# Optimization experiments

Hardware: AMD Instinct MI355X
Metric: run time of the kernel (lower is better)

Reference implementation:

```python
import jax, jax.numpy as jnp
import numpy as np

B, SEQ, VOCAB = 128, 200, 1400
D = 256          # input_size == hidden_size
H = 256
NCLS = 128


def _p(key, shape, scale=0.05):
    return jax.random.normal(key, shape, dtype=jnp.float32) * scale


def setup_inputs() -> dict:
    key = jax.random.key(0)
    ks = jax.random.split(key, 24)
    inp = {
        "inputs": jax.random.uniform(ks[0], (B, SEQ, VOCAB), dtype=jnp.float32),
        "timestamps": jax.random.uniform(ks[1], (B, SEQ), dtype=jnp.float32),
        "emb": _p(ks[2], (VOCAB, D)),
        # TimeLSTM 1
        "Wall1_w": _p(ks[3], (4 * H, D)), "Wall1_b": _p(ks[4], (4 * H,)),
        "Uall1_w": _p(ks[5], (4 * H, H)), "Uall1_b": _p(ks[6], (4 * H,)),
        "Wd1_w": _p(ks[7], (H, H)), "Wd1_b": _p(ks[8], (H,)),
        # TimeLSTM 2
        "Wall2_w": _p(ks[9], (4 * H, D)), "Wall2_b": _p(ks[10], (4 * H,)),
        "Uall2_w": _p(ks[11], (4 * H, H)), "Uall2_b": _p(ks[12], (4 * H,)),
        "Wd2_w": _p(ks[13], (H, H)), "Wd2_b": _p(ks[14], (H,)),
        # attention / output heads
        "wa_w": _p(ks[15], (1, H)),
        "Wb_w": _p(ks[16], (H, H)),
        "Wout_w": _p(ks[17], (NCLS, H)),
        # initial states (torch.randn in original forward)
        "h01": jax.random.normal(ks[18], (B, H), dtype=jnp.float32),
        "c01": jax.random.normal(ks[19], (B, H), dtype=jnp.float32),
        "h02": jax.random.normal(ks[20], (B, H), dtype=jnp.float32),
        "c02": jax.random.normal(ks[21], (B, H), dtype=jnp.float32),
    }
    return inp


def _time_lstm(embedded, timestamps, h0, c0, Wall_w, Wall_b, Uall_w, Uall_b, Wd_w, Wd_b):
    # Precompute the input projection for all steps (one big GEMM).
    # NOTE: original code applies W_all to h and U_all to x.
    ux = jnp.einsum('bsd,ed->sbe', embedded, Uall_w) + Uall_b  # [seq, b, 4h]
    ts = jnp.swapaxes(timestamps, 0, 1)[:, :, None]            # [seq, b, 1]

    def step(carry, xs):
        h, c = carry
        ux_s, t_s = xs
        c_s1 = jnp.tanh(c @ Wd_w.T + Wd_b)
        c_adj = c - c_s1 + c_s1 * t_s
        gates = jax.nn.sigmoid(h @ Wall_w.T + Wall_b + ux_s)   # all 4 gates sigmoid (incl. c_tmp)
        f, i, o, c_tmp = jnp.split(gates, 4, axis=1)
        c_new = f * c_adj + i * c_tmp
        h_new = o * jnp.tanh(c_new)
        return (h_new, c_new), h_new

    _, hs = jax.lax.scan(step, (h0, c0), (ux, ts))
    return jnp.swapaxes(hs, 0, 1)  # [b, seq, h]


def reference(inputs, timestamps, emb,
              Wall1_w, Wall1_b, Uall1_w, Uall1_b, Wd1_w, Wd1_b,
              Wall2_w, Wall2_b, Uall2_w, Uall2_b, Wd2_w, Wd2_b,
              wa_w, Wb_w, Wout_w, h01, c01, h02, c02):
    embedded = jnp.einsum('bsv,vd->bsd', inputs, emb)  # [b, seq, d]
    out1 = _time_lstm(embedded, timestamps, h01, c01,
                      Wall1_w, Wall1_b, Uall1_w, Uall1_b, Wd1_w, Wd1_b)
    E = jnp.einsum('bsh,h->bs', out1, wa_w[0])
    alpha = jax.nn.softmax(E, axis=1)                  # [b, seq]
    out2 = _time_lstm(embedded, timestamps, h02, c02,
                      Wall2_w, Wall2_b, Uall2_w, Uall2_b, Wd2_w, Wd2_b)
    Beta = jnp.tanh(jnp.einsum('bsh,kh->bsk', out2, Wb_w))  # [b, seq, h]
    ctx = jnp.sum(embedded * Beta * alpha[:, :, None], axis=1)  # [b, h]
    return ctx @ Wout_w.T  # [b, num_classes]
```

## Files before the change

kernel.cpp:

```cpp
#include <hip/hip_runtime.h>

typedef unsigned short u16;
typedef unsigned long long u64;
typedef __attribute__((ext_vector_type(8))) short bf16x8;
typedef __attribute__((ext_vector_type(4))) float f32x4;
typedef __attribute__((ext_vector_type(4))) unsigned short us4;

#define MFMA(a,b,c) __builtin_amdgcn_mfma_f32_16x16x32_bf16((a),(b),(c),0,0,0)
#define KEEP(x) asm volatile("" : "+v"(x))


static __device__ __forceinline__ u16 f2b(float f){
  unsigned u = __float_as_uint(f);
  u += 0x7fffu + ((u >> 16) & 1u);
  return (u16)(u >> 16);
}
static __device__ __forceinline__ float sigm(float x){ return 1.0f/(1.0f+__expf(-x)); }
static __device__ __forceinline__ float tanhx(float x){
  x = fminf(fmaxf(x, -15.f), 15.f);
  float e = __expf(-2.f*x);
  return (1.f - e)/(1.f + e);
}
static __device__ __forceinline__ void gl16(const void* g, void* l){
  __builtin_amdgcn_global_load_lds((const __attribute__((address_space(1))) void*)g,
                                   (__attribute__((address_space(3))) void*)l, 16, 0, 0);
}

__global__ __launch_bounds__(256) void k_prep(
  const float* __restrict__ in0, u16* __restrict__ A0,
  const float* __restrict__ emb, u16* __restrict__ embT,
  const float* __restrict__ s0, const float* __restrict__ s1, const float* __restrict__ s2,
  const float* __restrict__ s3, const float* __restrict__ s4, const float* __restrict__ s5,
  const float* __restrict__ s6,
  u16* __restrict__ d0, u16* __restrict__ d1, u16* __restrict__ d2, u16* __restrict__ d3,
  u16* __restrict__ d4, u16* __restrict__ d5, u16* __restrict__ d6)
{
  int bx = blockIdx.x, tid = threadIdx.x;
  if (bx < 35200){
    long long i4 = (long long)bx*256 + tid;
    long long o = i4*4;
    int r = (int)(o / 1408);
    int c = (int)(o % 1408);
    us4 d;
    if (c + 4 <= 1400){
      f32x4 v = *(const f32x4*)&in0[(long long)r*1400 + c];
      d[0]=f2b(v[0]); d[1]=f2b(v[1]); d[2]=f2b(v[2]); d[3]=f2b(v[3]);
    } else {
      for (int k=0;k<4;k++){ int cc=c+k; d[k] = (cc<1400)? f2b(in0[(long long)r*1400+cc]) : (u16)0; }
    }
    *(us4*)&A0[(long long)r*1408 + c] = d;
  } else if (bx < 36608){
    int idx = (bx-35200)*256 + tid;
    int n = idx / 1408, k = idx % 1408;
    embT[idx] = (k < 1400) ? f2b(emb[(long long)k*256 + n]) : (u16)0;
  } else {
    long long q = (long long)(bx-36608)*256 + tid;
    const float* src; u16* dst; long long rel;
    if      (q < 65536)  { src=s0; dst=d0; rel=q; }
    else if (q < 131072) { src=s1; dst=d1; rel=q-65536; }
    else if (q < 196608) { src=s2; dst=d2; rel=q-131072; }
    else if (q < 262144) { src=s3; dst=d3; rel=q-196608; }
    else if (q < 278528) { src=s4; dst=d4; rel=q-262144; }
    else if (q < 294912) { src=s5; dst=d5; rel=q-278528; }
    else                 { src=s6; dst=d6; rel=q-294912; }
    long long o = rel*4;
    f32x4 v = *(const f32x4*)&src[o];
    us4 d; d[0]=f2b(v[0]); d[1]=f2b(v[1]); d[2]=f2b(v[2]); d[3]=f2b(v[3]);
    *(us4*)&dst[o] = d;
  }
}

__global__ __launch_bounds__(256) void k_init(float* __restrict__ E, float* __restrict__ ctx){
  int i = blockIdx.x*256 + threadIdx.x;
  if (i < 25600) E[i] = 0.f;
  else ctx[i-25600] = 0.f;
}

template<int EPI>
__global__ __launch_bounds__(256) void k_gemm(const u16* __restrict__ A, const u16* __restrict__ Bt,
    int N, int K,
    float* __restrict__ Cf, u16* __restrict__ Cb,
    const float* __restrict__ bias1, const float* __restrict__ bias2,
    const u16* __restrict__ Bt2, float* __restrict__ Cf2,
    const float* __restrict__ bias3, const float* __restrict__ bias4,
    const float* __restrict__ emb, const float* __restrict__ alpha)
{
  __shared__ __align__(16) u16 As[128*64];
  __shared__ __align__(16) u16 Bs[128*64];
  __shared__ float red[2][128];
  const int tid = threadIdx.x;
  const int l = tid & 63, w = tid >> 6;
  const int quad = l >> 4, lb = l & 15;
  const int wr = w >> 1, wc = w & 1;
  const long long m0 = (long long)blockIdx.x * 128;
  int n0 = blockIdx.y * 128;
  if (EPI==4 && blockIdx.y >= 8){
    Bt = Bt2; Cf = Cf2; bias1 = bias3; bias2 = bias4; n0 = (blockIdx.y-8)*128;
  }

  f32x4 acc[4][4];
  #pragma unroll
  for (int i=0;i<4;i++)
    #pragma unroll
    for (int j=0;j<4;j++) acc[i][j] = (f32x4){0.f,0.f,0.f,0.f};

  for (int kk = 0; kk < K; kk += 64){
    #pragma unroll
    for (int it=0; it<4; ++it){
      int slot = it*256 + tid;
      int m = slot >> 3;
      int q = (slot & 7) ^ (m & 7);
      gl16(A + (m0+m)*K + kk + q*8, &As[slot*8]);
    }
    #pragma unroll
    for (int it=0; it<4; ++it){
      int slot = it*256 + tid;
      int m = slot >> 3;
      int q = (slot & 7) ^ (m & 7);
      gl16(Bt + (long long)(n0+m)*K + kk + q*8, &Bs[slot*8]);
    }
    __syncthreads();
    #pragma unroll
    for (int ks=0; ks<2; ++ks){
      int kq = quad + ks*4;
      bf16x8 af[4], bfr[4];
      #pragma unroll
      for (int i=0;i<4;i++){ int m = wr*64 + i*16 + lb; af[i]  = *(const bf16x8*)&As[m*64 + ((kq ^ (m&7))*8)]; }
      #pragma unroll
      for (int j=0;j<4;j++){ int n = wc*64 + j*16 + lb; bfr[j] = *(const bf16x8*)&Bs[n*64 + ((kq ^ (n&7))*8)]; }
      #pragma unroll
      for (int i=0;i<4;i++)
        #pragma unroll
        for (int j=0;j<4;j++)
          acc[i][j] = MFMA(af[i], bfr[j], acc[i][j]);
    }
    __syncthreads();
  }

  if (EPI==5){
    const int b0 = (int)(m0 / 200);
    red[tid>>7][tid&127] = 0.f;
    __syncthreads();
    #pragma unroll
    for (int i=0;i<4;i++){
      #pragma unroll
      for (int j=0;j<4;j++){
        int col = wc*64 + j*16 + lb;
        #pragma unroll
        for (int r=0;r<4;r++){
          long long row = m0 + wr*64 + i*16 + quad*4 + r;
          long long o = row*N + n0 + col;
          float v = emb[o] * tanhx(acc[i][j][r]) * alpha[row];
          atomicAdd(&red[(int)(row/200) - b0][col], v);
        }
      }
    }
    __syncthreads();
    int bl = tid >> 7, col = tid & 127;
    int bb = b0 + bl;
    if (bb < 128) atomicAdd(&Cf[bb*256 + n0 + col], red[bl][col]);
    return;
  }

  #pragma unroll
  for (int i=0;i<4;i++){
    #pragma unroll
    for (int j=0;j<4;j++){
      int col = n0 + wc*64 + j*16 + lb;
      #pragma unroll
      for (int r=0;r<4;r++){
        long long row = m0 + wr*64 + i*16 + quad*4 + r;
        long long o = row*N + col;
        float v = acc[i][j][r];
        if (EPI==1){ Cf[o]=v; Cb[o]=f2b(v); }
        else { Cf[o] = v + bias1[col] + bias2[col]; }
      }
    }
  }
}

__global__ __launch_bounds__(256,1) void k_scan(
  const u16* __restrict__ Wall1, const u16* __restrict__ Wd1, const float* __restrict__ Wd1b,
  const float* __restrict__ ux1, const float* __restrict__ h01, const float* __restrict__ c01,
  const u16* __restrict__ Wall2, const u16* __restrict__ Wd2, const float* __restrict__ Wd2b,
  const float* __restrict__ ux2, const float* __restrict__ h02, const float* __restrict__ c02,
  const float* __restrict__ ts, const float* __restrict__ wa,
  float* __restrict__ E, u16* __restrict__ out2,
  u16* __restrict__ hx, u16* __restrict__ cx, int* __restrict__ seqw)
{
  __shared__ __align__(16) u16 hb[16][264];
  __shared__ __align__(16) u16 cb[16][264];
  const int bi = blockIdx.x;
  const int lstm = bi >> 5;
  const int bc   = (bi >> 2) & 7;
  const int jw   = bi & 3;
  const int grp  = bi >> 2;
  const u16* Wall  = lstm ? Wall2 : Wall1;
  const u16* Wd    = lstm ? Wd2   : Wd1;
  const float* Wdb = lstm ? Wd2b  : Wd1b;
  const float* ux  = lstm ? ux2   : ux1;
  const float* h0  = lstm ? h02   : h01;
  const float* c0  = lstm ? c02   : c01;

  const int tid = threadIdx.x;
  const int l = tid & 63, w = tid >> 6;
  const int quad = l >> 4, lb = l & 15;
  const int bg = bc*16 + lb;
  const int jwave = jw*64 + w*16;
  const int jlane = jwave + quad*4;
  const int bb = tid >> 4, jj = tid & 15, j0 = jj*16;
  const int wjw = jj >> 2;

  bf16x8 wfA[4][8], wdA[8];
  #pragma unroll
  for (int g=0; g<4; ++g)
    #pragma unroll
    for (int kk=0; kk<8; ++kk){
      wfA[g][kk] = *(const bf16x8*)&Wall[(long long)(g*256 + jwave + lb)*256 + kk*32 + quad*8];
      KEEP(wfA[g][kk]);
    }
  #pragma unroll
  for (int kk=0; kk<8; ++kk){
    wdA[kk] = *(const bf16x8*)&Wd[(long long)(jwave + lb)*256 + kk*32 + quad*8];
    KEEP(wdA[kk]);
  }

  f32x4 bcs  = *(const f32x4*)&Wdb[jlane];
  f32x4 wav  = *(const f32x4*)&wa[jlane];
  f32x4 creg = *(const f32x4*)&c0[(long long)bg*256 + jlane];

  {
    #pragma unroll
    for (int kq=0; kq<4; ++kq){
      f32x4 hv = *(const f32x4*)&h0[(long long)(bc*16+bb)*256 + j0 + kq*4];
      f32x4 cv = *(const f32x4*)&c0[(long long)(bc*16+bb)*256 + j0 + kq*4];
      us4 hp, cp;
      #pragma unroll
      for (int r=0;r<4;++r){ hp[r]=f2b(hv[r]); cp[r]=f2b(cv[r]); }
      *(us4*)&hb[bb][j0+kq*4] = hp;
      *(us4*)&cb[bb][j0+kq*4] = cp;
    }
  }
  __syncthreads();

  f32x4 uxr[4];
  #pragma unroll
  for (int g=0; g<4; ++g)
    uxr[g] = *(const f32x4*)&ux[(long long)bg*200*1024 + g*256 + jlane];
  float tcur = ts[(long long)bg*200];

  for (int s=0; s<200; ++s){
    f32x4 ad = bcs;
    #pragma unroll
    for (int kk=0;kk<8;++kk){
      bf16x8 cf = *(const bf16x8*)&cb[lb][kk*32 + quad*8];
      ad = MFMA(wdA[kk], cf, ad);
    }
    f32x4 ag[4];
    #pragma unroll
    for (int g=0; g<4; ++g) ag[g] = uxr[g];
    #pragma unroll
    for (int kk=0;kk<8;++kk){
      bf16x8 hf = *(const bf16x8*)&hb[lb][kk*32 + quad*8];
      #pragma unroll
      for (int g=0; g<4; ++g) ag[g] = MFMA(wfA[g][kk], hf, ag[g]);
    }
    f32x4 hn; us4 hp, cp;
    #pragma unroll
    for (int r=0;r<4;++r){
      float cs1 = tanhx(ad[r]);
      float cadj = creg[r] + cs1*(tcur - 1.0f);
      float fg = sigm(ag[0][r]);
      float ig = sigm(ag[1][r]);
      float og = sigm(ag[2][r]);
      float cg = sigm(ag[3][r]);
      float cn = fg*cadj + ig*cg;
      float hv = og*tanhx(cn);
      creg[r]=cn; hn[r]=hv;
      hp[r]=f2b(hv); cp[r]=f2b(cn);
    }
    if (lstm==0){
      float e = hn[0]*wav[0] + hn[1]*wav[1] + hn[2]*wav[2] + hn[3]*wav[3];
      e += __shfl_xor(e, 16, 64);
      e += __shfl_xor(e, 32, 64);
      if (l < 16) atomicAdd(&E[(long long)bg*200 + s], e);
    } else {
      *(us4*)&out2[((long long)bg*200 + s)*256 + jlane] = hp;
    }
    if (s < 199){
      const int slot = (s+1)&1;
      u64 hv64, cv64;
      __builtin_memcpy(&hv64,&hp,8); __builtin_memcpy(&cv64,&cp,8);
      long long xbase = ((long long)(slot*16 + grp)*16 + lb)*256 + jlane;
      __hip_atomic_store((u64*)&hx[xbase], hv64, __ATOMIC_RELAXED, __HIP_MEMORY_SCOPE_AGENT);
      __hip_atomic_store((u64*)&cx[xbase], cv64, __ATOMIC_RELAXED, __HIP_MEMORY_SCOPE_AGENT);
      __syncthreads();
      if (tid == 0)
        __hip_atomic_store(&seqw[(slot*16+grp)*4 + jw], s+1, __ATOMIC_RELAXED, __HIP_MEMORY_SCOPE_AGENT);
      #pragma unroll
      for (int g=0; g<4; ++g)
        uxr[g] = *(const f32x4*)&ux[((long long)bg*200 + s+1)*1024 + g*256 + jlane];
      float tnext = ts[(long long)bg*200 + s+1];
      *(us4*)&hb[lb][jlane] = hp;
      *(us4*)&cb[lb][jlane] = cp;
      if (wjw != jw){
        const int* sp = &seqw[(slot*16+grp)*4 + wjw];
        while (__hip_atomic_load(sp, __ATOMIC_RELAXED, __HIP_MEMORY_SCOPE_AGENT) != s+1)
          __builtin_amdgcn_s_sleep(1);
        long long rbase = ((long long)(slot*16 + grp)*16 + bb)*256 + j0;
        u64 hvv[4], cvv[4];
        #pragma unroll
        for (int kq=0;kq<4;++kq){
          hvv[kq] = __hip_atomic_load((const u64*)&hx[rbase + kq*4], __ATOMIC_RELAXED, __HIP_MEMORY_SCOPE_AGENT);
          cvv[kq] = __hip_atomic_load((const u64*)&cx[rbase + kq*4], __ATOMIC_RELAXED, __HIP_MEMORY_SCOPE_AGENT);
        }
        #pragma unroll
        for (int kq=0;kq<4;++kq){
          *(u64*)&hb[bb][j0+kq*4] = hvv[kq];
          *(u64*)&cb[bb][j0+kq*4] = cvv[kq];
        }
      }
      tcur = tnext;
      __syncthreads();
    }
  }
}

__global__ __launch_bounds__(256) void k_attn(const float* __restrict__ E, float* __restrict__ alpha){
  __shared__ float buf[256];
  int b = blockIdx.x, tid = threadIdx.x;
  float Ev = (tid < 200) ? E[(long long)b*200 + tid] : -1e30f;
  buf[tid]=Ev; __syncthreads();
  for (int st=128; st>0; st>>=1){ if (tid<st) buf[tid]=fmaxf(buf[tid],buf[tid+st]); __syncthreads(); }
  float mx = buf[0]; __syncthreads();
  float e = (tid<200)? __expf(Ev-mx) : 0.f;
  buf[tid]=e; __syncthreads();
  for (int st=128; st>0; st>>=1){ if (tid<st) buf[tid]+=buf[tid+st]; __syncthreads(); }
  float sm = buf[0];
  if (tid<200) alpha[(long long)b*200+tid] = e/sm;
}

__global__ __launch_bounds__(128) void k_out(const float* __restrict__ ctx, const float* __restrict__ Wout,
                                             float* __restrict__ out){
  __shared__ float cs[256];
  int b = blockIdx.x, t = threadIdx.x;
  cs[t] = ctx[b*256+t]; cs[t+128] = ctx[b*256+t+128];
  __syncthreads();
  const float* wr = Wout + (long long)t*256;
  float a0=0,a1=0,a2=0,a3=0;
  for (int j=0;j<256;j+=4){
    f32x4 v = *(const f32x4*)&wr[j];
    a0+=v[0]*cs[j]; a1+=v[1]*cs[j+1]; a2+=v[2]*cs[j+2]; a3+=v[3]*cs[j+3];
  }
  out[(long long)b*128 + t] = (a0+a1)+(a2+a3);
}

extern "C" void kernel_launch(void* const* d_in, const int* in_sizes, int n_in,
                              void* d_out, int out_size, void* d_ws, size_t ws_size,
                              hipStream_t stream)
{
  (void)in_sizes; (void)n_in; (void)out_size; (void)ws_size;
  const float* inputs = (const float*)d_in[0];
  const float* tstamp = (const float*)d_in[1];
  const float* emb    = (const float*)d_in[2];
  const float* Wall1w = (const float*)d_in[3];
  const float* Wall1b = (const float*)d_in[4];
  const float* Uall1w = (const float*)d_in[5];
  const float* Uall1b = (const float*)d_in[6];
  const float* Wd1w   = (const float*)d_in[7];
  const float* Wd1b   = (const float*)d_in[8];
  const float* Wall2w = (const float*)d_in[9];
  const float* Wall2b = (const float*)d_in[10];
  const float* Uall2w = (const float*)d_in[11];
  const float* Uall2b = (const float*)d_in[12];
  const float* Wd2w   = (const float*)d_in[13];
  const float* Wd2b   = (const float*)d_in[14];
  const float* wa     = (const float*)d_in[15];
  const float* Wbw    = (const float*)d_in[16];
  const float* Woutw  = (const float*)d_in[17];
  const float* h01    = (const float*)d_in[18];
  const float* c01    = (const float*)d_in[19];
  const float* h02    = (const float*)d_in[20];
  const float* c02    = (const float*)d_in[21];

  char* ws = (char*)d_ws;
  float* ux1   = (float*)(ws + 0);
  float* ux2   = (float*)(ws + 104857600LL);
  float* embF  = (float*)(ws + 209715200LL);
  u16*   embB  = (u16*)  (ws + 235929600LL);
  char*  scr   =          ws + 249036800LL;
  u16*   A0    = (u16*)scr;
  u16*   out2  = (u16*)  (scr + 0);
  float* alpha = (float*)(scr + 39321600LL);
  float* ctx   = (float*)(scr + 39424000LL);
  float* E     = (float*)(scr + 39555072LL);
  u16*   hx    = (u16*)  (scr + 39657472LL);
  u16*   cx    = (u16*)  (scr + 39919616LL);
  int*   seqw  = (int*)  (scr + 40181760LL);
  u16* embT    = (u16*)(ws + 321126400LL);
  u16* Wall1B  = (u16*)(ws + 321847296LL);
  u16* Wall2B  = (u16*)(ws + 322371584LL);
  u16* Uall1B  = (u16*)(ws + 322895872LL);
  u16* Uall2B  = (u16*)(ws + 323420160LL);
  u16* Wd1B    = (u16*)(ws + 323944448LL);
  u16* Wd2B    = (u16*)(ws + 324075520LL);
  u16* WbB     = (u16*)(ws + 324206592LL);

  k_prep<<<37824, 256, 0, stream>>>(inputs, A0, emb, embT,
                                    Wall1w, Wall2w, Uall1w, Uall2w, Wd1w, Wd2w, Wbw,
                                    Wall1B, Wall2B, Uall1B, Uall2B, Wd1B, Wd2B, WbB);
  k_gemm<1><<<dim3(200,2), 256, 0, stream>>>(A0, embT, 256, 1408, embF, embB,
                                             nullptr, nullptr, nullptr, nullptr,
                                             nullptr, nullptr, nullptr, nullptr);
  k_gemm<4><<<dim3(200,16), 256, 0, stream>>>(embB, Uall1B, 1024, 256, ux1, nullptr,
                                              Uall1b, Wall1b,
                                              Uall2B, ux2, Uall2b, Wall2b,
                                              nullptr, nullptr);
  k_init<<<228, 256, 0, stream>>>(E, ctx);
  k_scan<<<64, 256, 0, stream>>>(Wall1B, Wd1B, Wd1b, ux1, h01, c01,
                                 Wall2B, Wd2B, Wd2b, ux2, h02, c02,
                                 tstamp, wa, E, out2, hx, cx, seqw);
  k_attn<<<128, 256, 0, stream>>>(E, alpha);
  k_gemm<5><<<dim3(200,2), 256, 0, stream>>>(out2, WbB, 256, 256, ctx, nullptr,
                                             nullptr, nullptr, nullptr, nullptr,
                                             nullptr, nullptr, embF, alpha);
  k_out<<<128, 128, 0, stream>>>(ctx, Woutw, (float*)d_out);
}
```

Measured before the change: 1.140 ms.

## Place scan blocks by XCD for local-cache exchange and store ux in bf16

The scan kernel now reads each block's XCC ID and assigns batch groups so that the four cooperating blocks share an XCD when possible. Those blocks exchange h and c state through workgroup-scope atomics that stay in the local L2, with a bounded spin that falls back to an agent-scope mirror. The ux projections are written in bf16 with biases folded in, which halves that traffic, and the next step's ux is prefetched earlier in the loop. The aim is lower per-step cross-block synchronisation latency in the 200-step recurrence. The cost is extra atomics, duplicated payload writes, and reliance on XCD co-residency and on cache-scope behaviour that is not guaranteed.

```diff
diff --git a/kernel.cpp b/kernel.cpp
--- a/kernel.cpp
+++ b/kernel.cpp
@@ -14,6 +14,9 @@
   unsigned u = __float_as_uint(f);
   u += 0x7fffu + ((u >> 16) & 1u);
   return (u16)(u >> 16);
+}
+static __device__ __forceinline__ float b2f(u16 v){
+  return __uint_as_float(((unsigned)v) << 16);
 }
 static __device__ __forceinline__ float sigm(float x){ return 1.0f/(1.0f+__expf(-x)); }
 static __device__ __forceinline__ float tanhx(float x){
@@ -70,10 +73,12 @@
   }
 }
 
-__global__ __launch_bounds__(256) void k_init(float* __restrict__ E, float* __restrict__ ctx){
+__global__ __launch_bounds__(256) void k_init(float* __restrict__ E, float* __restrict__ ctx,
+                                              int* __restrict__ cnts){
   int i = blockIdx.x*256 + threadIdx.x;
-  if (i < 25600) E[i] = 0.f;
-  else ctx[i-25600] = 0.f;
+  if (i < 32768) E[i] = 0.f;
+  else if (i < 65536) ctx[i-32768] = 0.f;
+  else if (i < 65568) cnts[i-65536] = 0;
 }
 
 template<int EPI>
@@ -81,7 +86,7 @@
     int N, int K,
     float* __restrict__ Cf, u16* __restrict__ Cb,
     const float* __restrict__ bias1, const float* __restrict__ bias2,
-    const u16* __restrict__ Bt2, float* __restrict__ Cf2,
+    const u16* __restrict__ Bt2, u16* __restrict__ Cb2,
     const float* __restrict__ bias3, const float* __restrict__ bias4,
     const float* __restrict__ emb, const float* __restrict__ alpha)
 {
@@ -94,8 +99,8 @@
   const int wr = w >> 1, wc = w & 1;
   const long long m0 = (long long)blockIdx.x * 128;
   int n0 = blockIdx.y * 128;
-  if (EPI==4 && blockIdx.y >= 8){
-    Bt = Bt2; Cf = Cf2; bias1 = bias3; bias2 = bias4; n0 = (blockIdx.y-8)*128;
+  if (EPI==6 && blockIdx.y >= 8){
+    Bt = Bt2; Cb = Cb2; bias1 = bias3; bias2 = bias4; n0 = (blockIdx.y-8)*128;
   }
 
   f32x4 acc[4][4];
@@ -173,7 +178,7 @@
         long long o = row*N + col;
         float v = acc[i][j][r];
         if (EPI==1){ Cf[o]=v; Cb[o]=f2b(v); }
-        else { Cf[o] = v + bias1[col] + bias2[col]; }
+        else if (EPI==6){ Cb[o] = f2b(v + bias1[col] + bias2[col]); }
       }
     }
   }
@@ -181,28 +186,61 @@
 
 __global__ __launch_bounds__(256,1) void k_scan(
   const u16* __restrict__ Wall1, const u16* __restrict__ Wd1, const float* __restrict__ Wd1b,
-  const float* __restrict__ ux1, const float* __restrict__ h01, const float* __restrict__ c01,
+  const u16* __restrict__ ux1, const float* __restrict__ h01, const float* __restrict__ c01,
   const u16* __restrict__ Wall2, const u16* __restrict__ Wd2, const float* __restrict__ Wd2b,
-  const float* __restrict__ ux2, const float* __restrict__ h02, const float* __restrict__ c02,
+  const u16* __restrict__ ux2, const float* __restrict__ h02, const float* __restrict__ c02,
   const float* __restrict__ ts, const float* __restrict__ wa,
   float* __restrict__ E, u16* __restrict__ out2,
-  u16* __restrict__ hx, u16* __restrict__ cx, int* __restrict__ seqw)
+  u64* __restrict__ pay, unsigned* __restrict__ flg,
+  u64* __restrict__ mpay, unsigned* __restrict__ mflg,
+  int* __restrict__ cntp, int* __restrict__ totalp, int* __restrict__ fbp)
 {
   __shared__ __align__(16) u16 hb[16][264];
   __shared__ __align__(16) u16 cb[16][264];
+  __shared__ int bcast[3];
+  __shared__ int lok;
+
   const int bi = blockIdx.x;
   const int lstm = bi >> 5;
-  const int bc   = (bi >> 2) & 7;
-  const int jw   = bi & 3;
-  const int grp  = bi >> 2;
+  const int tid = threadIdx.x;
+
+  if (tid == 0){
+    int xcd;
+    asm volatile("s_getreg_b32 %0, hwreg(HW_REG_XCC_ID)" : "=s"(xcd));
+    xcd &= 7;
+    int slot = __hip_atomic_fetch_add(&cntp[lstm*8+xcd], 1, __ATOMIC_RELAXED, __HIP_MEMORY_SCOPE_AGENT);
+    __hip_atomic_fetch_add(totalp, 1, __ATOMIC_RELAXED, __HIP_MEMORY_SCOPE_AGENT);
+    while (__hip_atomic_load(totalp, __ATOMIC_RELAXED, __HIP_MEMORY_SCOPE_AGENT) < 64)
+      __builtin_amdgcn_s_sleep(8);
+    int c[8];
+    #pragma unroll
+    for (int x=0;x<8;x++)
+      c[x] = __hip_atomic_load(&cntp[lstm*8+x], __ATOMIC_RELAXED, __HIP_MEMORY_SCOPE_AGENT);
+    int myq = slot>>2, bc, jw, lg;
+    if (myq < (c[xcd]>>2)){
+      int base=0;
+      for (int x=0;x<xcd;x++) base += c[x]>>2;
+      bc = base + myq; jw = slot&3; lg = 1;
+    } else {
+      int C=0;
+      for (int x=0;x<8;x++) C += c[x]>>2;
+      int fb = __hip_atomic_fetch_add(&fbp[lstm], 1, __ATOMIC_RELAXED, __HIP_MEMORY_SCOPE_AGENT);
+      bc = C + (fb>>2); jw = fb&3; lg = 0;
+    }
+    bcast[0]=bc; bcast[1]=jw; bcast[2]=lg; lok = lg;
+  }
+  __syncthreads();
+  const int bc = bcast[0];
+  const int jw = bcast[1];
+  const int grp = lstm*8 + bc;
+
   const u16* Wall  = lstm ? Wall2 : Wall1;
   const u16* Wd    = lstm ? Wd2   : Wd1;
   const float* Wdb = lstm ? Wd2b  : Wd1b;
-  const float* ux  = lstm ? ux2   : ux1;
+  const u16* ux    = lstm ? ux2   : ux1;
   const float* h0  = lstm ? h02   : h01;
   const float* c0  = lstm ? c02   : c01;
 
-  const int tid = threadIdx.x;
   const int l = tid & 63, w = tid >> 6;
   const int quad = l >> 4, lb = l & 15;
   const int bg = bc*16 + lb;
@@ -229,36 +267,44 @@
   f32x4 wav  = *(const f32x4*)&wa[jlane];
   f32x4 creg = *(const f32x4*)&c0[(long long)bg*256 + jlane];
 
-  {
-    #pragma unroll
-    for (int kq=0; kq<4; ++kq){
-      f32x4 hv = *(const f32x4*)&h0[(long long)(bc*16+bb)*256 + j0 + kq*4];
-      f32x4 cv = *(const f32x4*)&c0[(long long)(bc*16+bb)*256 + j0 + kq*4];
-      us4 hp, cp;
-      #pragma unroll
-      for (int r=0;r<4;++r){ hp[r]=f2b(hv[r]); cp[r]=f2b(cv[r]); }
-      *(us4*)&hb[bb][j0+kq*4] = hp;
-      *(us4*)&cb[bb][j0+kq*4] = cp;
-    }
+  #pragma unroll
+  for (int kq=0; kq<4; ++kq){
+    f32x4 hv = *(const f32x4*)&h0[(long long)(bc*16+bb)*256 + j0 + kq*4];
+    f32x4 cv = *(const f32x4*)&c0[(long long)(bc*16+bb)*256 + j0 + kq*4];
+    us4 hp0, cp0;
+    #pragma unroll
+    for (int r=0;r<4;++r){ hp0[r]=f2b(hv[r]); cp0[r]=f2b(cv[r]); }
+    *(us4*)&hb[bb][j0+kq*4] = hp0;
+    *(us4*)&cb[bb][j0+kq*4] = cp0;
   }
   __syncthreads();
 
-  f32x4 uxr[4];
+  us4 uxr[4];
   #pragma unroll
   for (int g=0; g<4; ++g)
-    uxr[g] = *(const f32x4*)&ux[(long long)bg*200*1024 + g*256 + jlane];
+    uxr[g] = *(const us4*)&ux[(long long)bg*200*1024 + g*256 + jlane];
   float tcur = ts[(long long)bg*200];
 
   for (int s=0; s<200; ++s){
+    const int lk = lok;
+    f32x4 ag[4];
+    #pragma unroll
+    for (int g=0; g<4; ++g)
+      #pragma unroll
+      for (int r=0; r<4; ++r) ag[g][r] = b2f(uxr[g][r]);
+    float tnx = 0.f;
+    if (s < 199){
+      #pragma unroll
+      for (int g=0; g<4; ++g)
+        uxr[g] = *(const us4*)&ux[((long long)bg*200 + s+1)*1024 + g*256 + jlane];
+      tnx = ts[(long long)bg*200 + s+1];
+    }
     f32x4 ad = bcs;
     #pragma unroll
     for (int kk=0;kk<8;++kk){
       bf16x8 cf = *(const bf16x8*)&cb[lb][kk*32 + quad*8];
       ad = MFMA(wdA[kk], cf, ad);
     }
-    f32x4 ag[4];
-    #pragma unroll
-    for (int g=0; g<4; ++g) ag[g] = uxr[g];
     #pragma unroll
     for (int kk=0;kk<8;++kk){
       bf16x8 hf = *(const bf16x8*)&hb[lb][kk*32 + quad*8];
@@ -283,44 +329,84 @@
       float e = hn[0]*wav[0] + hn[1]*wav[1] + hn[2]*wav[2] + hn[3]*wav[3];
       e += __shfl_xor(e, 16, 64);
       e += __shfl_xor(e, 32, 64);
-      if (l < 16) atomicAdd(&E[(long long)bg*200 + s], e);
+      if (l < 16)
+        __hip_atomic_fetch_add(&E[(long long)bg*256 + s], e, __ATOMIC_RELAXED, __HIP_MEMORY_SCOPE_AGENT);
     } else {
       *(us4*)&out2[((long long)bg*200 + s)*256 + jlane] = hp;
     }
     if (s < 199){
       const int slot = (s+1)&1;
-      u64 hv64, cv64;
-      __builtin_memcpy(&hv64,&hp,8); __builtin_memcpy(&cv64,&cp,8);
-      long long xbase = ((long long)(slot*16 + grp)*16 + lb)*256 + jlane;
-      __hip_atomic_store((u64*)&hx[xbase], hv64, __ATOMIC_RELAXED, __HIP_MEMORY_SCOPE_AGENT);
-      __hip_atomic_store((u64*)&cx[xbase], cv64, __ATOMIC_RELAXED, __HIP_MEMORY_SCOPE_AGENT);
+      const int fbase = (slot*16+grp)*16;
+      u64 h64, c64;
+      __builtin_memcpy(&h64,&hp,8); __builtin_memcpy(&c64,&cp,8);
+      long long W = ((long long)(slot*16+grp)*16 + lb)*128 + ((jlane>>2)<<1);
+      if (lk){
+        __hip_atomic_store(&pay[W],   h64, __ATOMIC_RELAXED, __HIP_MEMORY_SCOPE_WORKGROUP);
+        __hip_atomic_store(&pay[W+1], c64, __ATOMIC_RELAXED, __HIP_MEMORY_SCOPE_WORKGROUP);
+      }
+      __hip_atomic_store(&mpay[W],   h64, __ATOMIC_RELAXED, __HIP_MEMORY_SCOPE_AGENT);
+      __hip_atomic_store(&mpay[W+1], c64, __ATOMIC_RELAXED, __HIP_MEMORY_SCOPE_AGENT);
       __syncthreads();
-      if (tid == 0)
-        __hip_atomic_store(&seqw[(slot*16+grp)*4 + jw], s+1, __ATOMIC_RELAXED, __HIP_MEMORY_SCOPE_AGENT);
-      #pragma unroll
-      for (int g=0; g<4; ++g)
-        uxr[g] = *(const f32x4*)&ux[((long long)bg*200 + s+1)*1024 + g*256 + jlane];
-      float tnext = ts[(long long)bg*200 + s+1];
+      if (tid == 0){
+        if (lk) __hip_atomic_store(&flg[fbase+jw], (unsigned)(s+1), __ATOMIC_RELAXED, __HIP_MEMORY_SCOPE_WORKGROUP);
+        __hip_atomic_store(&mflg[fbase+jw], (unsigned)(s+1), __ATOMIC_RELAXED, __HIP_MEMORY_SCOPE_AGENT);
+      }
       *(us4*)&hb[lb][jlane] = hp;
       *(us4*)&cb[lb][jlane] = cp;
-      if (wjw != jw){
-        const int* sp = &seqw[(slot*16+grp)*4 + wjw];
-        while (__hip_atomic_load(sp, __ATOMIC_RELAXED, __HIP_MEMORY_SCOPE_AGENT) != s+1)
-          __builtin_amdgcn_s_sleep(1);
-        long long rbase = ((long long)(slot*16 + grp)*16 + bb)*256 + j0;
-        u64 hvv[4], cvv[4];
-        #pragma unroll
-        for (int kq=0;kq<4;++kq){
-          hvv[kq] = __hip_atomic_load((const u64*)&hx[rbase + kq*4], __ATOMIC_RELAXED, __HIP_MEMORY_SCOPE_AGENT);
-          cvv[kq] = __hip_atomic_load((const u64*)&cx[rbase + kq*4], __ATOMIC_RELAXED, __HIP_MEMORY_SCOPE_AGENT);
+      if (tid < 4 && tid != jw){
+        const unsigned tgt = (unsigned)(s+1);
+        bool ok = false;
+        if (lk){
+          for (int it=0; it<3000; ++it){
+            unsigned v = __hip_atomic_fetch_add(&flg[fbase+tid], 65536u, __ATOMIC_RELAXED, __HIP_MEMORY_SCOPE_WORKGROUP);
+            if ((v & 0xFFFFu) == tgt){ ok = true; break; }
+            __builtin_amdgcn_s_sleep(2);
+          }
+          if (!ok) lok = 0;
         }
-        #pragma unroll
-        for (int kq=0;kq<4;++kq){
-          *(u64*)&hb[bb][j0+kq*4] = hvv[kq];
-          *(u64*)&cb[bb][j0+kq*4] = cvv[kq];
+        if (!ok){
+          while (__hip_atomic_load(&mflg[fbase+tid], __ATOMIC_RELAXED, __HIP_MEMORY_SCOPE_AGENT) != tgt)
+            __builtin_amdgcn_s_sleep(2);
         }
       }
-      tcur = tnext;
+      __syncthreads();
+      if (wjw != jw){
+        const int lk2 = lok;
+        long long R = ((long long)(slot*16+grp)*16 + bb)*128 + jj*8;
+        u64 h0v,c0v,h1v,c1v,h2v,c2v,h3v,c3v;
+        if (lk2){
+          u64 a = (u64)(unsigned long long)(uintptr_t)&pay[R];
+          u64 z = 0;
+          asm volatile(
+            "global_atomic_add_x2 %[o0], %[a], %[z], off sc0\n\t"
+            "global_atomic_add_x2 %[o1], %[a], %[z], off offset:8 sc0\n\t"
+            "global_atomic_add_x2 %[o2], %[a], %[z], off offset:16 sc0\n\t"
+            "global_atomic_add_x2 %[o3], %[a], %[z], off offset:24 sc0\n\t"
+            "global_atomic_add_x2 %[o4], %[a], %[z], off offset:32 sc0\n\t"
+            "global_atomic_add_x2 %[o5], %[a], %[z], off offset:40 sc0\n\t"
+            "global_atomic_add_x2 %[o6], %[a], %[z], off offset:48 sc0\n\t"
+            "global_atomic_add_x2 %[o7], %[a], %[z], off offset:56 sc0\n\t"
+            "s_waitcnt vmcnt(0)"
+            : [o0]"=v"(h0v), [o1]"=v"(c0v), [o2]"=v"(h1v), [o3]"=v"(c1v),
+              [o4]"=v"(h2v), [o5]"=v"(c2v), [o6]"=v"(h3v), [o7]"=v"(c3v)
+            : [a]"v"(a), [z]"v"(z)
+            : "memory");
+        } else {
+          h0v = __hip_atomic_load(&mpay[R+0], __ATOMIC_RELAXED, __HIP_MEMORY_SCOPE_AGENT);
+          c0v = __hip_atomic_load(&mpay[R+1], __ATOMIC_RELAXED, __HIP_MEMORY_SCOPE_AGENT);
+          h1v = __hip_atomic_load(&mpay[R+2], __ATOMIC_RELAXED, __HIP_MEMORY_SCOPE_AGENT);
+          c1v = __hip_atomic_load(&mpay[R+3], __ATOMIC_RELAXED, __HIP_MEMORY_SCOPE_AGENT);
+          h2v = __hip_atomic_load(&mpay[R+4], __ATOMIC_RELAXED, __HIP_MEMORY_SCOPE_AGENT);
+          c2v = __hip_atomic_load(&mpay[R+5], __ATOMIC_RELAXED, __HIP_MEMORY_SCOPE_AGENT);
+          h3v = __hip_atomic_load(&mpay[R+6], __ATOMIC_RELAXED, __HIP_MEMORY_SCOPE_AGENT);
+          c3v = __hip_atomic_load(&mpay[R+7], __ATOMIC_RELAXED, __HIP_MEMORY_SCOPE_AGENT);
+        }
+        *(u64*)&hb[bb][j0+ 0] = h0v;  *(u64*)&cb[bb][j0+ 0] = c0v;
+        *(u64*)&hb[bb][j0+ 4] = h1v;  *(u64*)&cb[bb][j0+ 4] = c1v;
+        *(u64*)&hb[bb][j0+ 8] = h2v;  *(u64*)&cb[bb][j0+ 8] = c2v;
+        *(u64*)&hb[bb][j0+12] = h3v;  *(u64*)&cb[bb][j0+12] = c3v;
+      }
+      tcur = tnx;
       __syncthreads();
     }
   }
@@ -329,7 +415,7 @@
 __global__ __launch_bounds__(256) void k_attn(const float* __restrict__ E, float* __restrict__ alpha){
   __shared__ float buf[256];
   int b = blockIdx.x, tid = threadIdx.x;
-  float Ev = (tid < 200) ? E[(long long)b*200 + tid] : -1e30f;
+  float Ev = (tid < 200) ? E[(long long)b*256 + tid] : -1e30f;
   buf[tid]=Ev; __syncthreads();
   for (int st=128; st>0; st>>=1){ if (tid<st) buf[tid]=fmaxf(buf[tid],buf[tid+st]); __syncthreads(); }
   float mx = buf[0]; __syncthreads();
@@ -384,27 +470,33 @@
   const float* c02    = (const float*)d_in[21];
 
   char* ws = (char*)d_ws;
-  float* ux1   = (float*)(ws + 0);
-  float* ux2   = (float*)(ws + 104857600LL);
-  float* embF  = (float*)(ws + 209715200LL);
-  u16*   embB  = (u16*)  (ws + 235929600LL);
-  char*  scr   =          ws + 249036800LL;
+  u16*   ux1   = (u16*)  (ws + 0);
+  u16*   ux2   = (u16*)  (ws + 52428800LL);
+  float* embF  = (float*)(ws + 104857600LL);
+  u16*   embB  = (u16*)  (ws + 131072000LL);
+  char*  scr   =          ws + 144179200LL;
   u16*   A0    = (u16*)scr;
   u16*   out2  = (u16*)  (scr + 0);
-  float* alpha = (float*)(scr + 39321600LL);
-  float* ctx   = (float*)(scr + 39424000LL);
-  float* E     = (float*)(scr + 39555072LL);
-  u16*   hx    = (u16*)  (scr + 39657472LL);
-  u16*   cx    = (u16*)  (scr + 39919616LL);
-  int*   seqw  = (int*)  (scr + 40181760LL);
-  u16* embT    = (u16*)(ws + 321126400LL);
-  u16* Wall1B  = (u16*)(ws + 321847296LL);
-  u16* Wall2B  = (u16*)(ws + 322371584LL);
-  u16* Uall1B  = (u16*)(ws + 322895872LL);
-  u16* Uall2B  = (u16*)(ws + 323420160LL);
-  u16* Wd1B    = (u16*)(ws + 323944448LL);
-  u16* Wd2B    = (u16*)(ws + 324075520LL);
-  u16* WbB     = (u16*)(ws + 324206592LL);
+  float* E     = (float*)(scr + 13107200LL);
+  float* ctx   = (float*)(scr + 13238272LL);
+  float* alpha = (float*)(scr + 13369344LL);
+  u64*   pay   = (u64*)  (scr + 13471744LL);
+  unsigned* flg= (unsigned*)(scr + 13996032LL);
+  u64*   mpay  = (u64*)  (scr + 13998080LL);
+  unsigned* mflg=(unsigned*)(scr + 14522368LL);
+  int*   cnts  = (int*)  (scr + 14524416LL);
+  u16* embT    = (u16*)(ws + 216268800LL);
+  u16* Wall1B  = (u16*)(ws + 216989696LL);
+  u16* Wall2B  = (u16*)(ws + 217513984LL);
+  u16* Uall1B  = (u16*)(ws + 218038272LL);
+  u16* Uall2B  = (u16*)(ws + 218562560LL);
+  u16* Wd1B    = (u16*)(ws + 219086848LL);
+  u16* Wd2B    = (u16*)(ws + 219217920LL);
+  u16* WbB     = (u16*)(ws + 219348992LL);
+
+  int* cntp   = cnts;
+  int* totalp = cnts + 16;
+  int* fbp    = cnts + 17;
 
   k_prep<<<37824, 256, 0, stream>>>(inputs, A0, emb, embT,
                                     Wall1w, Wall2w, Uall1w, Uall2w, Wd1w, Wd2w, Wbw,
@@ -412,14 +504,15 @@
   k_gemm<1><<<dim3(200,2), 256, 0, stream>>>(A0, embT, 256, 1408, embF, embB,
                                              nullptr, nullptr, nullptr, nullptr,
                                              nullptr, nullptr, nullptr, nullptr);
-  k_gemm<4><<<dim3(200,16), 256, 0, stream>>>(embB, Uall1B, 1024, 256, ux1, nullptr,
+  k_gemm<6><<<dim3(200,16), 256, 0, stream>>>(embB, Uall1B, 1024, 256, nullptr, ux1,
                                               Uall1b, Wall1b,
                                               Uall2B, ux2, Uall2b, Wall2b,
                                               nullptr, nullptr);
-  k_init<<<228, 256, 0, stream>>>(E, ctx);
+  k_init<<<257, 256, 0, stream>>>(E, ctx, cnts);
   k_scan<<<64, 256, 0, stream>>>(Wall1B, Wd1B, Wd1b, ux1, h01, c01,
                                  Wall2B, Wd2B, Wd2b, ux2, h02, c02,
-                                 tstamp, wa, E, out2, hx, cx, seqw);
+                                 tstamp, wa, E, out2,
+                                 pay, flg, mpay, mflg, cntp, totalp, fbp);
   k_attn<<<128, 256, 0, stream>>>(E, alpha);
   k_gemm<5><<<dim3(200,2), 256, 0, stream>>>(out2, WbB, 256, 256, ctx, nullptr,
                                              nullptr, nullptr, nullptr, nullptr,
```

After: 1.826 ms. 1.6x slower.

## Keep LSTM state fragments in registers, store ux as bf16, rework cross-block exchange

Applied to the files above, without the earlier changes.

The recurrent scan kernel no longer stages h/c in shared memory. Each lane loads its MFMA B-fragments straight from a global exchange buffer after polling per-sibling flags with a ballot, which removes LDS writes, a barrier and the per-thread spin loops. The ux projection is now written and read as bf16 instead of fp32, halving that traffic, and the next step's ux is prefetched earlier in the loop. E is padded to stride 256. The cost is more redundant global loads per lane from the exchange buffer and lower precision for the gate preactivation input.

```diff
diff --git a/kernel.cpp b/kernel.cpp
--- a/kernel.cpp
+++ b/kernel.cpp
@@ -14,6 +14,9 @@
   unsigned u = __float_as_uint(f);
   u += 0x7fffu + ((u >> 16) & 1u);
   return (u16)(u >> 16);
+}
+static __device__ __forceinline__ float b2f(u16 v){
+  return __uint_as_float(((unsigned)v) << 16);
 }
 static __device__ __forceinline__ float sigm(float x){ return 1.0f/(1.0f+__expf(-x)); }
 static __device__ __forceinline__ float tanhx(float x){
@@ -72,8 +75,8 @@
 
 __global__ __launch_bounds__(256) void k_init(float* __restrict__ E, float* __restrict__ ctx){
   int i = blockIdx.x*256 + threadIdx.x;
-  if (i < 25600) E[i] = 0.f;
-  else ctx[i-25600] = 0.f;
+  if (i < 32768) E[i] = 0.f;
+  else ctx[i-32768] = 0.f;
 }
 
 template<int EPI>
@@ -81,7 +84,7 @@
     int N, int K,
     float* __restrict__ Cf, u16* __restrict__ Cb,
     const float* __restrict__ bias1, const float* __restrict__ bias2,
-    const u16* __restrict__ Bt2, float* __restrict__ Cf2,
+    const u16* __restrict__ Bt2, u16* __restrict__ Cb2,
     const float* __restrict__ bias3, const float* __restrict__ bias4,
     const float* __restrict__ emb, const float* __restrict__ alpha)
 {
@@ -94,8 +97,8 @@
   const int wr = w >> 1, wc = w & 1;
   const long long m0 = (long long)blockIdx.x * 128;
   int n0 = blockIdx.y * 128;
-  if (EPI==4 && blockIdx.y >= 8){
-    Bt = Bt2; Cf = Cf2; bias1 = bias3; bias2 = bias4; n0 = (blockIdx.y-8)*128;
+  if (EPI==6 && blockIdx.y >= 8){
+    Bt = Bt2; Cb = Cb2; bias1 = bias3; bias2 = bias4; n0 = (blockIdx.y-8)*128;
   }
 
   f32x4 acc[4][4];
@@ -173,7 +176,7 @@
         long long o = row*N + col;
         float v = acc[i][j][r];
         if (EPI==1){ Cf[o]=v; Cb[o]=f2b(v); }
-        else { Cf[o] = v + bias1[col] + bias2[col]; }
+        else if (EPI==6){ Cb[o] = f2b(v + bias1[col] + bias2[col]); }
       }
     }
   }
@@ -181,15 +184,13 @@
 
 __global__ __launch_bounds__(256,1) void k_scan(
   const u16* __restrict__ Wall1, const u16* __restrict__ Wd1, const float* __restrict__ Wd1b,
-  const float* __restrict__ ux1, const float* __restrict__ h01, const float* __restrict__ c01,
+  const u16* __restrict__ ux1, const float* __restrict__ h01, const float* __restrict__ c01,
   const u16* __restrict__ Wall2, const u16* __restrict__ Wd2, const float* __restrict__ Wd2b,
-  const float* __restrict__ ux2, const float* __restrict__ h02, const float* __restrict__ c02,
+  const u16* __restrict__ ux2, const float* __restrict__ h02, const float* __restrict__ c02,
   const float* __restrict__ ts, const float* __restrict__ wa,
   float* __restrict__ E, u16* __restrict__ out2,
-  u16* __restrict__ hx, u16* __restrict__ cx, int* __restrict__ seqw)
+  u16* __restrict__ mpay, unsigned* __restrict__ mflg)
 {
-  __shared__ __align__(16) u16 hb[16][264];
-  __shared__ __align__(16) u16 cb[16][264];
   const int bi = blockIdx.x;
   const int lstm = bi >> 5;
   const int bc   = (bi >> 2) & 7;
@@ -198,7 +199,7 @@
   const u16* Wall  = lstm ? Wall2 : Wall1;
   const u16* Wd    = lstm ? Wd2   : Wd1;
   const float* Wdb = lstm ? Wd2b  : Wd1b;
-  const float* ux  = lstm ? ux2   : ux1;
+  const u16* ux    = lstm ? ux2   : ux1;
   const float* h0  = lstm ? h02   : h01;
   const float* c0  = lstm ? c02   : c01;
 
@@ -208,8 +209,7 @@
   const int bg = bc*16 + lb;
   const int jwave = jw*64 + w*16;
   const int jlane = jwave + quad*4;
-  const int bb = tid >> 4, jj = tid & 15, j0 = jj*16;
-  const int wjw = jj >> 2;
+  const int sib = (l < 3) ? (l + (l >= jw ? 1 : 0)) : 0;
 
   bf16x8 wfA[4][8], wdA[8];
   #pragma unroll
@@ -229,42 +229,48 @@
   f32x4 wav  = *(const f32x4*)&wa[jlane];
   f32x4 creg = *(const f32x4*)&c0[(long long)bg*256 + jlane];
 
-  {
-    #pragma unroll
-    for (int kq=0; kq<4; ++kq){
-      f32x4 hv = *(const f32x4*)&h0[(long long)(bc*16+bb)*256 + j0 + kq*4];
-      f32x4 cv = *(const f32x4*)&c0[(long long)(bc*16+bb)*256 + j0 + kq*4];
-      us4 hp, cp;
-      #pragma unroll
-      for (int r=0;r<4;++r){ hp[r]=f2b(hv[r]); cp[r]=f2b(cv[r]); }
-      *(us4*)&hb[bb][j0+kq*4] = hp;
-      *(us4*)&cb[bb][j0+kq*4] = cp;
-    }
-  }
-  __syncthreads();
-
-  f32x4 uxr[4];
+  bf16x8 hfr[8], cfr[8];
+  #pragma unroll
+  for (int kk=0; kk<8; ++kk){
+    const float* hs = &h0[(long long)bg*256 + kk*32 + quad*8];
+    const float* cs = &c0[(long long)bg*256 + kk*32 + quad*8];
+    f32x4 ha = *(const f32x4*)hs, hb4 = *(const f32x4*)(hs+4);
+    f32x4 ca = *(const f32x4*)cs, cb4 = *(const f32x4*)(cs+4);
+    union { u16 u[8]; bf16x8 v; } th, tc;
+    #pragma unroll
+    for (int r=0;r<4;++r){
+      th.u[r]=f2b(ha[r]); th.u[4+r]=f2b(hb4[r]);
+      tc.u[r]=f2b(ca[r]); tc.u[4+r]=f2b(cb4[r]);
+    }
+    hfr[kk]=th.v; cfr[kk]=tc.v;
+  }
+
+  us4 uxr[4];
   #pragma unroll
   for (int g=0; g<4; ++g)
-    uxr[g] = *(const f32x4*)&ux[(long long)bg*200*1024 + g*256 + jlane];
+    uxr[g] = *(const us4*)&ux[(long long)bg*200*1024 + g*256 + jlane];
   float tcur = ts[(long long)bg*200];
 
   for (int s=0; s<200; ++s){
+    f32x4 ag[4];
+    #pragma unroll
+    for (int g=0; g<4; ++g)
+      #pragma unroll
+      for (int r=0; r<4; ++r) ag[g][r] = b2f(uxr[g][r]);
+    float tnx = 0.f;
+    if (s < 199){
+      #pragma unroll
+      for (int g=0; g<4; ++g)
+        uxr[g] = *(const us4*)&ux[((long long)bg*200 + s+1)*1024 + g*256 + jlane];
+      tnx = ts[(long long)bg*200 + s+1];
+    }
     f32x4 ad = bcs;
     #pragma unroll
-    for (int kk=0;kk<8;++kk){
-      bf16x8 cf = *(const bf16x8*)&cb[lb][kk*32 + quad*8];
-      ad = MFMA(wdA[kk], cf, ad);
-    }
-    f32x4 ag[4];
-    #pragma unroll
-    for (int g=0; g<4; ++g) ag[g] = uxr[g];
-    #pragma unroll
-    for (int kk=0;kk<8;++kk){
-      bf16x8 hf = *(const bf16x8*)&hb[lb][kk*32 + quad*8];
-      #pragma unroll
-      for (int g=0; g<4; ++g) ag[g] = MFMA(wfA[g][kk], hf, ag[g]);
-    }
+    for (int kk=0;kk<8;++kk) ad = MFMA(wdA[kk], cfr[kk], ad);
+    #pragma unroll
+    for (int kk=0;kk<8;++kk)
+      #pragma unroll
+      for (int g=0; g<4; ++g) ag[g] = MFMA(wfA[g][kk], hfr[kk], ag[g]);
     f32x4 hn; us4 hp, cp;
     #pragma unroll
     for (int r=0;r<4;++r){
@@ -279,49 +285,45 @@
       creg[r]=cn; hn[r]=hv;
       hp[r]=f2b(hv); cp[r]=f2b(cn);
     }
+    tcur = tnx;
     if (lstm==0){
       float e = hn[0]*wav[0] + hn[1]*wav[1] + hn[2]*wav[2] + hn[3]*wav[3];
       e += __shfl_xor(e, 16, 64);
       e += __shfl_xor(e, 32, 64);
-      if (l < 16) atomicAdd(&E[(long long)bg*200 + s], e);
+      if (l < 16) atomicAdd(&E[(long long)bg*256 + s], e);
     } else {
       *(us4*)&out2[((long long)bg*200 + s)*256 + jlane] = hp;
     }
     if (s < 199){
       const int slot = (s+1)&1;
-      u64 hv64, cv64;
-      __builtin_memcpy(&hv64,&hp,8); __builtin_memcpy(&cv64,&cp,8);
-      long long xbase = ((long long)(slot*16 + grp)*16 + lb)*256 + jlane;
-      __hip_atomic_store((u64*)&hx[xbase], hv64, __ATOMIC_RELAXED, __HIP_MEMORY_SCOPE_AGENT);
-      __hip_atomic_store((u64*)&cx[xbase], cv64, __ATOMIC_RELAXED, __HIP_MEMORY_SCOPE_AGENT);
+      const long long base = ((long long)(slot*16+grp)*16 + lb)*512;
+      const int fbase = (slot*16+grp)*64;
+      u64 h64, c64;
+      __builtin_memcpy(&h64,&hp,8); __builtin_memcpy(&c64,&cp,8);
+      __hip_atomic_store((u64*)&mpay[base + jlane],       h64, __ATOMIC_RELAXED, __HIP_MEMORY_SCOPE_AGENT);
+      __hip_atomic_store((u64*)&mpay[base + 256 + jlane], c64, __ATOMIC_RELAXED, __HIP_MEMORY_SCOPE_AGENT);
       __syncthreads();
       if (tid == 0)
-        __hip_atomic_store(&seqw[(slot*16+grp)*4 + jw], s+1, __ATOMIC_RELAXED, __HIP_MEMORY_SCOPE_AGENT);
-      #pragma unroll
-      for (int g=0; g<4; ++g)
-        uxr[g] = *(const f32x4*)&ux[((long long)bg*200 + s+1)*1024 + g*256 + jlane];
-      float tnext = ts[(long long)bg*200 + s+1];
-      *(us4*)&hb[lb][jlane] = hp;
-      *(us4*)&cb[lb][jlane] = cp;
-      if (wjw != jw){
-        const int* sp = &seqw[(slot*16+grp)*4 + wjw];
-        while (__hip_atomic_load(sp, __ATOMIC_RELAXED, __HIP_MEMORY_SCOPE_AGENT) != s+1)
-          __builtin_amdgcn_s_sleep(1);
-        long long rbase = ((long long)(slot*16 + grp)*16 + bb)*256 + j0;
-        u64 hvv[4], cvv[4];
-        #pragma unroll
-        for (int kq=0;kq<4;++kq){
-          hvv[kq] = __hip_atomic_load((const u64*)&hx[rbase + kq*4], __ATOMIC_RELAXED, __HIP_MEMORY_SCOPE_AGENT);
-          cvv[kq] = __hip_atomic_load((const u64*)&cx[rbase + kq*4], __ATOMIC_RELAXED, __HIP_MEMORY_SCOPE_AGENT);
-        }
-        #pragma unroll
-        for (int kq=0;kq<4;++kq){
-          *(u64*)&hb[bb][j0+kq*4] = hvv[kq];
-          *(u64*)&cb[bb][j0+kq*4] = cvv[kq];
-        }
+        __hip_atomic_store(&mflg[fbase + jw*16], (unsigned)(s+1), __ATOMIC_RELAXED, __HIP_MEMORY_SCOPE_AGENT);
+      const unsigned tgt = (unsigned)(s+1);
+      for (;;){
+        unsigned fv = tgt;
+        if (l < 3)
+          fv = __hip_atomic_load(&mflg[fbase + sib*16], __ATOMIC_RELAXED, __HIP_MEMORY_SCOPE_AGENT);
+        if ((__ballot(fv == tgt) & 7ULL) == 7ULL) break;
+        __builtin_amdgcn_s_sleep(1);
       }
-      tcur = tnext;
-      __syncthreads();
+      #pragma unroll
+      for (int kk=0;kk<8;++kk){
+        long long o = base + kk*32 + quad*8;
+        u64 hlo = __hip_atomic_load((const u64*)&mpay[o],      __ATOMIC_RELAXED, __HIP_MEMORY_SCOPE_AGENT);
+        u64 hhi = __hip_atomic_load((const u64*)&mpay[o+4],    __ATOMIC_RELAXED, __HIP_MEMORY_SCOPE_AGENT);
+        u64 clo = __hip_atomic_load((const u64*)&mpay[o+256],  __ATOMIC_RELAXED, __HIP_MEMORY_SCOPE_AGENT);
+        u64 chi = __hip_atomic_load((const u64*)&mpay[o+260],  __ATOMIC_RELAXED, __HIP_MEMORY_SCOPE_AGENT);
+        union { u64 q[2]; bf16x8 v; } th, tc;
+        th.q[0]=hlo; th.q[1]=hhi; tc.q[0]=clo; tc.q[1]=chi;
+        hfr[kk]=th.v; cfr[kk]=tc.v;
+      }
     }
   }
 }
@@ -329,7 +331,7 @@
 __global__ __launch_bounds__(256) void k_attn(const float* __restrict__ E, float* __restrict__ alpha){
   __shared__ float buf[256];
   int b = blockIdx.x, tid = threadIdx.x;
-  float Ev = (tid < 200) ? E[(long long)b*200 + tid] : -1e30f;
+  float Ev = (tid < 200) ? E[(long long)b*256 + tid] : -1e30f;
   buf[tid]=Ev; __syncthreads();
   for (int st=128; st>0; st>>=1){ if (tid<st) buf[tid]=fmaxf(buf[tid],buf[tid+st]); __syncthreads(); }
   float mx = buf[0]; __syncthreads();
@@ -384,27 +386,26 @@
   const float* c02    = (const float*)d_in[21];
 
   char* ws = (char*)d_ws;
-  float* ux1   = (float*)(ws + 0);
-  float* ux2   = (float*)(ws + 104857600LL);
-  float* embF  = (float*)(ws + 209715200LL);
-  u16*   embB  = (u16*)  (ws + 235929600LL);
-  char*  scr   =          ws + 249036800LL;
+  u16*   ux1   = (u16*)  (ws + 0);
+  u16*   ux2   = (u16*)  (ws + 52428800LL);
+  float* embF  = (float*)(ws + 104857600LL);
+  u16*   embB  = (u16*)  (ws + 131072000LL);
+  char*  scr   =          ws + 144179200LL;
   u16*   A0    = (u16*)scr;
   u16*   out2  = (u16*)  (scr + 0);
-  float* alpha = (float*)(scr + 39321600LL);
-  float* ctx   = (float*)(scr + 39424000LL);
-  float* E     = (float*)(scr + 39555072LL);
-  u16*   hx    = (u16*)  (scr + 39657472LL);
-  u16*   cx    = (u16*)  (scr + 39919616LL);
-  int*   seqw  = (int*)  (scr + 40181760LL);
-  u16* embT    = (u16*)(ws + 321126400LL);
-  u16* Wall1B  = (u16*)(ws + 321847296LL);
-  u16* Wall2B  = (u16*)(ws + 322371584LL);
-  u16* Uall1B  = (u16*)(ws + 322895872LL);
-  u16* Uall2B  = (u16*)(ws + 323420160LL);
-  u16* Wd1B    = (u16*)(ws + 323944448LL);
-  u16* Wd2B    = (u16*)(ws + 324075520LL);
-  u16* WbB     = (u16*)(ws + 324206592LL);
+  float* E     = (float*)(scr + 13107200LL);
+  float* ctx   = (float*)(scr + 13238272LL);
+  float* alpha = (float*)(scr + 13369344LL);
+  u16*   mpay  = (u16*)  (scr + 13471744LL);
+  unsigned* mflg=(unsigned*)(scr + 13996032LL);
+  u16* embT    = (u16*)(ws + 216268800LL);
+  u16* Wall1B  = (u16*)(ws + 216989696LL);
+  u16* Wall2B  = (u16*)(ws + 217513984LL);
+  u16* Uall1B  = (u16*)(ws + 218038272LL);
+  u16* Uall2B  = (u16*)(ws + 218562560LL);
+  u16* Wd1B    = (u16*)(ws + 219086848LL);
+  u16* Wd2B    = (u16*)(ws + 219217920LL);
+  u16* WbB     = (u16*)(ws + 219348992LL);
 
   k_prep<<<37824, 256, 0, stream>>>(inputs, A0, emb, embT,
                                     Wall1w, Wall2w, Uall1w, Uall2w, Wd1w, Wd2w, Wbw,
@@ -412,14 +413,14 @@
   k_gemm<1><<<dim3(200,2), 256, 0, stream>>>(A0, embT, 256, 1408, embF, embB,
                                              nullptr, nullptr, nullptr, nullptr,
                                              nullptr, nullptr, nullptr, nullptr);
-  k_gemm<4><<<dim3(200,16), 256, 0, stream>>>(embB, Uall1B, 1024, 256, ux1, nullptr,
+  k_gemm<6><<<dim3(200,16), 256, 0, stream>>>(embB, Uall1B, 1024, 256, nullptr, ux1,
                                               Uall1b, Wall1b,
                                               Uall2B, ux2, Uall2b, Wall2b,
                                               nullptr, nullptr);
-  k_init<<<228, 256, 0, stream>>>(E, ctx);
+  k_init<<<256, 256, 0, stream>>>(E, ctx);
   k_scan<<<64, 256, 0, stream>>>(Wall1B, Wd1B, Wd1b, ux1, h01, c01,
                                  Wall2B, Wd2B, Wd2b, ux2, h02, c02,
-                                 tstamp, wa, E, out2, hx, cx, seqw);
+                                 tstamp, wa, E, out2, mpay, mflg);
   k_attn<<<128, 256, 0, stream>>>(E, alpha);
   k_gemm<5><<<dim3(200,2), 256, 0, stream>>>(out2, WbB, 256, 256, ctx, nullptr,
                                              nullptr, nullptr, nullptr, nullptr,
```

Result: slower. 1.624 ms (+42.4%).
